# Performance work log

Hardware: AMD Instinct MI355X
Metric: run time of the kernel (lower is better)

The kernel has to match this reference:

```python
import jax, jax.numpy as jnp
import numpy as np

N_NODES = 50000
N_EDGES = 800000
D_FEAT = 128


def setup_inputs() -> dict:
    key = jax.random.key(0)
    k1, k2, k3, k4 = jax.random.split(key, 4)
    edge_index = jax.random.randint(k1, (2, N_EDGES), 0, N_NODES, dtype=jnp.int64 if jax.config.jax_enable_x64 else jnp.int32)
    edge_vals = jax.random.uniform(k2, (N_EDGES,), dtype=jnp.float32)
    features = jax.random.normal(k3, (N_NODES, D_FEAT), dtype=jnp.float32)
    bias = jax.random.normal(k4, (D_FEAT,), dtype=jnp.float32)
    return {"edge_index": edge_index, "edge_vals": edge_vals, "features": features, "bias": bias}


def reference(edge_index, edge_vals, features, bias):
    # SpMM: out[dst] += A[dst, src] * X[src], i.e. sparse adjacency @ dense features
    src = edge_index[0]
    dst = edge_index[1]
    msg = features[src] * edge_vals[:, None]          # [E, D] gather + scale
    out = jax.ops.segment_sum(msg, dst, num_segments=features.shape[0])  # [N, D] scatter-add
    return out + bias                                  # fused bias add
```

## Files before the change

kernel.cpp:

```cpp
#include <hip/hip_runtime.h>
#include <hip/hip_bf16.h>

#define D_FEAT 128
#define D4 (D_FEAT / 4)
#define BKT_SHIFT 7
#define BKT_NODES 128
#define NCHUNK 256
#define MAXBKT 512
#define MAXBSUM 128
#define CAP 3072

__global__ __launch_bounds__(256) void k1_hist_cvt(
        const int* __restrict__ dst, int E, int chunk, int nbkt,
        int* __restrict__ M, int Mpad,
        const float4* __restrict__ fin, __hip_bfloat162* __restrict__ fout,
        int n4) {
    int c = blockIdx.x;
    int tid = threadIdx.x;
    if (c < NCHUNK) {
        __shared__ int hist[MAXBKT];
        for (int i = tid; i < nbkt; i += 256) hist[i] = 0;
        __syncthreads();
        int lo = c * chunk;
        int hi = min(lo + chunk, E);
        for (int i = lo + tid; i < hi; i += 256)
            atomicAdd(&hist[dst[i] >> BKT_SHIFT], 1);
        __syncthreads();
        for (int i = tid; i < nbkt; i += 256)
            M[i * NCHUNK + c] = hist[i];
        if (c == 0) {
            for (int i = nbkt * NCHUNK + tid; i < Mpad; i += 256) M[i] = 0;
        }
    } else {
        int nb = gridDim.x - NCHUNK;
        int idx = (c - NCHUNK) * 256 + tid;
        int stride = nb * 256;
        for (int i = idx; i < n4; i += stride) {
            float4 f = fin[i];
            fout[2 * i + 0] = __float22bfloat162_rn(make_float2(f.x, f.y));
            fout[2 * i + 1] = __float22bfloat162_rn(make_float2(f.z, f.w));
        }
    }
}

__global__ __launch_bounds__(1024) void k2a_scan(int* __restrict__ M,
                                                 int* __restrict__ bsum) {
    __shared__ int s[1024];
    int tid = threadIdx.x;
    int j = blockIdx.x * 1024 + tid;
    int v = M[j];
    s[tid] = v;
    __syncthreads();
    for (int off = 1; off < 1024; off <<= 1) {
        int t = (tid >= off) ? s[tid - off] : 0;
        __syncthreads();
        s[tid] += t;
        __syncthreads();
    }
    M[j] = s[tid] - v;
    if (tid == 1023) bsum[blockIdx.x] = s[1023];
}

__device__ inline void scan_bsum_lds(const int* __restrict__ bsum, int nblk,
                                     int* sbs, int tid) {
    int v = 0;
    if (tid < MAXBSUM) {
        v = (tid < nblk) ? bsum[tid] : 0;
        sbs[tid] = v;
    }
    __syncthreads();
    for (int off = 1; off < MAXBSUM; off <<= 1) {
        int t = (tid < MAXBSUM && tid >= off) ? sbs[tid - off] : 0;
        __syncthreads();
        if (tid < MAXBSUM) sbs[tid] += t;
        __syncthreads();
    }
    if (tid < MAXBSUM) sbs[tid] -= v;
    __syncthreads();
}

__global__ __launch_bounds__(512) void k3_partition(
        const int* __restrict__ src, const int* __restrict__ dst,
        const float* __restrict__ vals, int E, int chunk, int nbkt, int nblk,
        const int* __restrict__ M, const int* __restrict__ bsum,
        int2* __restrict__ spackA) {
    __shared__ int sbs[MAXBSUM];
    __shared__ int lcur[MAXBKT];
    int c = blockIdx.x;
    int tid = threadIdx.x;
    scan_bsum_lds(bsum, nblk, sbs, tid);
    for (int i = tid; i < nbkt; i += 512) {
        int j = i * NCHUNK + c;
        lcur[i] = M[j] + sbs[j >> 10];
    }
    __syncthreads();
    int lo = c * chunk;
    int hi = min(lo + chunk, E);
    for (int i = lo + tid; i < hi; i += 512) {
        int d = dst[i];
        int s = src[i];
        float v = vals[i];
        int pos = atomicAdd(&lcur[d >> BKT_SHIFT], 1);
        spackA[pos] = make_int2((s & 0xFFFF) | ((d & (BKT_NODES - 1)) << 16),
                                __float_as_int(v));
    }
}

__global__ __launch_bounds__(1024) void k45_sort_gather(
        const int* __restrict__ M, const int* __restrict__ bsum, int nblk,
        const int2* __restrict__ spackA, int2* __restrict__ spackB,
        const __hip_bfloat162* __restrict__ feat,
        const float2* __restrict__ bias2, float2* __restrict__ out2,
        int N, int nbkt) {
    __shared__ int sbs[MAXBSUM];
    __shared__ int hist[BKT_NODES];
    __shared__ int sbuf[BKT_NODES];
    __shared__ int lcur[BKT_NODES];
    __shared__ int2 ls[CAP];
    int b = blockIdx.x;
    int tid = threadIdx.x;
    scan_bsum_lds(bsum, nblk, sbs, tid);
    int j0 = b * NCHUNK;
    int j1 = (b + 1) * NCHUNK;
    int base = M[j0] + sbs[j0 >> 10];
    int end  = M[j1] + sbs[j1 >> 10];
    int cnt = end - base;
    bool inlds = (cnt <= CAP);

    if (tid < BKT_NODES) hist[tid] = 0;
    __syncthreads();
    for (int i = tid; i < cnt; i += 1024)
        atomicAdd(&hist[(spackA[base + i].x >> 16) & (BKT_NODES - 1)], 1);
    __syncthreads();
    if (tid < BKT_NODES) sbuf[tid] = hist[tid];
    __syncthreads();
    for (int off = 1; off < BKT_NODES; off <<= 1) {
        int t = (tid < BKT_NODES && tid >= off) ? sbuf[tid - off] : 0;
        __syncthreads();
        if (tid < BKT_NODES) sbuf[tid] += t;
        __syncthreads();
    }
    if (tid < BKT_NODES) lcur[tid] = sbuf[tid] - hist[tid];
    __syncthreads();
    for (int i = tid; i < cnt; i += 1024) {
        int2 r = spackA[base + i];
        int p = atomicAdd(&lcur[(r.x >> 16) & (BKT_NODES - 1)], 1);
        if (inlds) ls[p] = r;
        else       spackB[base + p] = r;
    }
    __syncthreads();

    int wave = tid >> 6, lane = tid & 63;
    float2 bv = bias2[lane];
    for (int n = wave; n < BKT_NODES; n += 16) {
        int node = (b << BKT_SHIFT) + n;
        if (node >= N) break;
        int lbeg = sbuf[n] - hist[n];
        int lend = sbuf[n];
        float2 acc0 = bv;
        float2 acc1 = make_float2(0.f, 0.f);
        if (inlds) {
            for (int e0 = lbeg; e0 < lend; e0 += 8) {
                int2 p[8];
                __hip_bfloat162 h[8];
#pragma unroll
                for (int j = 0; j < 8; j++) p[j] = ls[min(e0 + j, lend - 1)];
#pragma unroll
                for (int j = 0; j < 8; j++)
                    h[j] = feat[(size_t)(p[j].x & 0xFFFF) * 64 + lane];
#pragma unroll
                for (int j = 0; j < 8; j++) {
                    float v = (e0 + j < lend) ? __int_as_float(p[j].y) : 0.f;
                    float2 f = __bfloat1622float2(h[j]);
                    if (j & 1) { acc1.x += v * f.x; acc1.y += v * f.y; }
                    else       { acc0.x += v * f.x; acc0.y += v * f.y; }
                }
            }
        } else {
            for (int e0 = lbeg; e0 < lend; e0 += 8) {
                int2 p[8];
                __hip_bfloat162 h[8];
#pragma unroll
                for (int j = 0; j < 8; j++)
                    p[j] = spackB[base + min(e0 + j, lend - 1)];
#pragma unroll
                for (int j = 0; j < 8; j++)
                    h[j] = feat[(size_t)(p[j].x & 0xFFFF) * 64 + lane];
#pragma unroll
                for (int j = 0; j < 8; j++) {
                    float v = (e0 + j < lend) ? __int_as_float(p[j].y) : 0.f;
                    float2 f = __bfloat1622float2(h[j]);
                    if (j & 1) { acc1.x += v * f.x; acc1.y += v * f.y; }
                    else       { acc0.x += v * f.x; acc0.y += v * f.y; }
                }
            }
        }
        acc0.x += acc1.x; acc0.y += acc1.y;
        out2[(size_t)node * 64 + lane] = acc0;
    }
}


__global__ void init_bias_kernel(float4* __restrict__ out,
                                 const float4* __restrict__ bias, int n4) {
    int i = blockIdx.x * blockDim.x + threadIdx.x;
    if (i < n4) out[i] = bias[i & (D4 - 1)];
}

__global__ void spmm_edge_kernel(const int* __restrict__ src,
                                 const int* __restrict__ dst,
                                 const float* __restrict__ vals,
                                 const float4* __restrict__ feat,
                                 float* __restrict__ out, int n_edges) {
    int tid = blockIdx.x * blockDim.x + threadIdx.x;
    int e = tid >> 5;
    int lane = tid & 31;
    if (e >= n_edges) return;
    int s = src[e];
    int d = dst[e];
    float v = vals[e];
    float4 f = feat[(size_t)s * D4 + lane];
    float* o = out + (size_t)d * D_FEAT + lane * 4;
    atomicAdd(o + 0, v * f.x);
    atomicAdd(o + 1, v * f.y);
    atomicAdd(o + 2, v * f.z);
    atomicAdd(o + 3, v * f.w);
}

extern "C" void kernel_launch(void* const* d_in, const int* in_sizes, int n_in,
                              void* d_out, int out_size, void* d_ws, size_t ws_size,
                              hipStream_t stream) {
    const int* edge_index = (const int*)d_in[0];
    const float* edge_vals = (const float*)d_in[1];
    const float* features  = (const float*)d_in[2];
    const float* bias      = (const float*)d_in[3];

    int E = in_sizes[1];
    int N = in_sizes[2] / D_FEAT;
    const int* src = edge_index;
    const int* dst = edge_index + E;
    float* out = (float*)d_out;

    int nbkt = (N + BKT_NODES - 1) >> BKT_SHIFT;
    int n4 = N * D_FEAT / 4;
    int chunk = (E + NCHUNK - 1) / NCHUNK;
    int Mpad = ((nbkt * NCHUNK + 1 + 1023) / 1024) * 1024;
    int nblk2 = Mpad / 1024;

    size_t fb_bytes = (size_t)N * D_FEAT * 2;
    size_t sp_bytes = (size_t)E * 8;
    size_t needed = fb_bytes + 2 * sp_bytes +
                    ((size_t)Mpad + nblk2) * 4;

    bool ok = (ws_size >= needed) && (N >= 1) && (N <= 65536) && (E >= 1) &&
              (in_sizes[3] == D_FEAT) && (nbkt <= MAXBKT) && (nblk2 <= MAXBSUM);

    if (ok) {
        char* wp = (char*)d_ws;
        __hip_bfloat162* fb16 = (__hip_bfloat162*)wp;  wp += fb_bytes;
        int2* spackA = (int2*)wp;                      wp += sp_bytes;
        int2* spackB = (int2*)wp;                      wp += sp_bytes;
        int* M       = (int*)wp;                       wp += (size_t)Mpad * 4;
        int* bsum    = (int*)wp;

        k1_hist_cvt<<<NCHUNK + 256, 256, 0, stream>>>(dst, E, chunk, nbkt,
                                                      M, Mpad,
                                                      (const float4*)features,
                                                      fb16, n4);
        k2a_scan<<<nblk2, 1024, 0, stream>>>(M, bsum);
        k3_partition<<<NCHUNK, 512, 0, stream>>>(src, dst, edge_vals, E, chunk,
                                                 nbkt, nblk2, M, bsum, spackA);
        k45_sort_gather<<<nbkt, 1024, 0, stream>>>(M, bsum, nblk2,
                                                   spackA, spackB,
                                                   fb16, (const float2*)bias,
                                                   (float2*)out, N, nbkt);
    } else {
        int no4 = out_size / 4;
        {
            int block = 256, grid = (no4 + block - 1) / block;
            init_bias_kernel<<<grid, block, 0, stream>>>((float4*)out,
                                                         (const float4*)bias, no4);
        }
        {
            int block = 256;
            long long total = (long long)E * 32;
            int grid = (int)((total + block - 1) / block);
            spmm_edge_kernel<<<grid, block, 0, stream>>>(src, dst, edge_vals,
                                                         (const float4*)features,
                                                         out, E);
        }
    }
}
```

Baseline: 146.0 us.

## Split wave into half-waves gathering 8-byte feature rows, use shuffle scans

In the gather phase each wave now splits into two 32-lane halves, and each half processes alternate edges. Each lane loads 4 bf16 features (8 bytes) instead of 2, and the halves are combined with a cross-half shuffle before the float4 store. This doubles the number of edges in flight per wave and widens memory transactions, at the cost of an extra reduction step. The LDS-based block scans of bucket sums and the per-node histogram are replaced with wave-level shuffle scans, which removes many barriers. The bf16 conversion also writes packed uint2 values.

Measured after the change: 144.1 us. No clear change (-1.3%).

```diff
diff --git a/kernel.cpp b/kernel.cpp
--- a/kernel.cpp
+++ b/kernel.cpp
@@ -10,10 +10,17 @@
 #define MAXBSUM 128
 #define CAP 3072
 
+__device__ inline unsigned pack_bf2(float lo, float hi) {
+    __hip_bfloat162 h = __float22bfloat162_rn(make_float2(lo, hi));
+    unsigned u;
+    __builtin_memcpy(&u, &h, 4);
+    return u;
+}
+
 __global__ __launch_bounds__(256) void k1_hist_cvt(
         const int* __restrict__ dst, int E, int chunk, int nbkt,
         int* __restrict__ M, int Mpad,
-        const float4* __restrict__ fin, __hip_bfloat162* __restrict__ fout,
+        const float4* __restrict__ fin, uint2* __restrict__ fout,
         int n4) {
     int c = blockIdx.x;
     int tid = threadIdx.x;
@@ -37,8 +44,10 @@
         int stride = nb * 256;
         for (int i = idx; i < n4; i += stride) {
             float4 f = fin[i];
-            fout[2 * i + 0] = __float22bfloat162_rn(make_float2(f.x, f.y));
-            fout[2 * i + 1] = __float22bfloat162_rn(make_float2(f.z, f.w));
+            uint2 o;
+            o.x = pack_bf2(f.x, f.y);
+            o.y = pack_bf2(f.z, f.w);
+            fout[i] = o;
         }
     }
 }
@@ -61,21 +70,21 @@
     if (tid == 1023) bsum[blockIdx.x] = s[1023];
 }
 
-__device__ inline void scan_bsum_lds(const int* __restrict__ bsum, int nblk,
-                                     int* sbs, int tid) {
-    int v = 0;
-    if (tid < MAXBSUM) {
-        v = (tid < nblk) ? bsum[tid] : 0;
-        sbs[tid] = v;
-    }
-    __syncthreads();
-    for (int off = 1; off < MAXBSUM; off <<= 1) {
-        int t = (tid < MAXBSUM && tid >= off) ? sbs[tid - off] : 0;
-        __syncthreads();
-        if (tid < MAXBSUM) sbs[tid] += t;
-        __syncthreads();
-    }
-    if (tid < MAXBSUM) sbs[tid] -= v;
+__device__ inline void scan_bsum_wave(const int* __restrict__ bsum, int nblk,
+                                      int* sbs, int tid) {
+    if (tid < 64) {
+        int i0 = 2 * tid, i1 = 2 * tid + 1;
+        int h0 = (i0 < nblk) ? bsum[i0] : 0;
+        int h1 = (i1 < nblk) ? bsum[i1] : 0;
+        int s = h0 + h1;
+        int v = s;
+        for (int off = 1; off < 64; off <<= 1) {
+            int t = __shfl_up(v, off, 64);
+            if (tid >= off) v += t;
+        }
+        sbs[i0] = v - s;
+        sbs[i1] = v - s + h0;
+    }
     __syncthreads();
 }
 
@@ -88,7 +97,7 @@
     __shared__ int lcur[MAXBKT];
     int c = blockIdx.x;
     int tid = threadIdx.x;
-    scan_bsum_lds(bsum, nblk, sbs, tid);
+    scan_bsum_wave(bsum, nblk, sbs, tid);
     for (int i = tid; i < nbkt; i += 512) {
         int j = i * NCHUNK + c;
         lcur[i] = M[j] + sbs[j >> 10];
@@ -109,8 +118,8 @@
 __global__ __launch_bounds__(1024) void k45_sort_gather(
         const int* __restrict__ M, const int* __restrict__ bsum, int nblk,
         const int2* __restrict__ spackA, int2* __restrict__ spackB,
-        const __hip_bfloat162* __restrict__ feat,
-        const float2* __restrict__ bias2, float2* __restrict__ out2,
+        const uint2* __restrict__ feat2,
+        const float4* __restrict__ bias4, float4* __restrict__ out4,
         int N, int nbkt) {
     __shared__ int sbs[MAXBSUM];
     __shared__ int hist[BKT_NODES];
@@ -119,7 +128,7 @@
     __shared__ int2 ls[CAP];
     int b = blockIdx.x;
     int tid = threadIdx.x;
-    scan_bsum_lds(bsum, nblk, sbs, tid);
+    scan_bsum_wave(bsum, nblk, sbs, tid);
     int j0 = b * NCHUNK;
     int j1 = (b + 1) * NCHUNK;
     int base = M[j0] + sbs[j0 >> 10];
@@ -132,15 +141,19 @@
     for (int i = tid; i < cnt; i += 1024)
         atomicAdd(&hist[(spackA[base + i].x >> 16) & (BKT_NODES - 1)], 1);
     __syncthreads();
-    if (tid < BKT_NODES) sbuf[tid] = hist[tid];
-    __syncthreads();
-    for (int off = 1; off < BKT_NODES; off <<= 1) {
-        int t = (tid < BKT_NODES && tid >= off) ? sbuf[tid - off] : 0;
-        __syncthreads();
-        if (tid < BKT_NODES) sbuf[tid] += t;
-        __syncthreads();
-    }
-    if (tid < BKT_NODES) lcur[tid] = sbuf[tid] - hist[tid];
+    if (tid < 64) {
+        int h0 = hist[2 * tid], h1 = hist[2 * tid + 1];
+        int s = h0 + h1;
+        int v = s;
+        for (int off = 1; off < 64; off <<= 1) {
+            int t = __shfl_up(v, off, 64);
+            if (tid >= off) v += t;
+        }
+        sbuf[2 * tid]     = v - h1;
+        sbuf[2 * tid + 1] = v;
+        lcur[2 * tid]     = v - s;
+        lcur[2 * tid + 1] = v - h1;
+    }
     __syncthreads();
     for (int i = tid; i < cnt; i += 1024) {
         int2 r = spackA[base + i];
@@ -151,52 +164,82 @@
     __syncthreads();
 
     int wave = tid >> 6, lane = tid & 63;
-    float2 bv = bias2[lane];
+    int half = lane >> 5;
+    int hl   = lane & 31;
+    float4 bv = bias4[hl];
     for (int n = wave; n < BKT_NODES; n += 16) {
         int node = (b << BKT_SHIFT) + n;
         if (node >= N) break;
-        int lbeg = sbuf[n] - hist[n];
         int lend = sbuf[n];
-        float2 acc0 = bv;
-        float2 acc1 = make_float2(0.f, 0.f);
+        int lbeg = lend - hist[n];
+        float4 acc0 = make_float4(0.f, 0.f, 0.f, 0.f);
+        float4 acc1 = make_float4(0.f, 0.f, 0.f, 0.f);
         if (inlds) {
-            for (int e0 = lbeg; e0 < lend; e0 += 8) {
+            for (int e0 = lbeg; e0 < lend; e0 += 16) {
                 int2 p[8];
-                __hip_bfloat162 h[8];
-#pragma unroll
-                for (int j = 0; j < 8; j++) p[j] = ls[min(e0 + j, lend - 1)];
+                uint2 h[8];
 #pragma unroll
                 for (int j = 0; j < 8; j++)
-                    h[j] = feat[(size_t)(p[j].x & 0xFFFF) * 64 + lane];
+                    p[j] = ls[min(e0 + 2 * j + half, lend - 1)];
+#pragma unroll
+                for (int j = 0; j < 8; j++)
+                    h[j] = feat2[(size_t)(p[j].x & 0xFFFF) * 32 + hl];
 #pragma unroll
                 for (int j = 0; j < 8; j++) {
-                    float v = (e0 + j < lend) ? __int_as_float(p[j].y) : 0.f;
-                    float2 f = __bfloat1622float2(h[j]);
-                    if (j & 1) { acc1.x += v * f.x; acc1.y += v * f.y; }
-                    else       { acc0.x += v * f.x; acc0.y += v * f.y; }
+                    float v = (e0 + 2 * j + half < lend) ? __int_as_float(p[j].y) : 0.f;
+                    __hip_bfloat162 blo, bhi;
+                    __builtin_memcpy(&blo, &h[j].x, 4);
+                    __builtin_memcpy(&bhi, &h[j].y, 4);
+                    float2 f01 = __bfloat1622float2(blo);
+                    float2 f23 = __bfloat1622float2(bhi);
+                    if (j & 1) {
+                        acc1.x += v * f01.x; acc1.y += v * f01.y;
+                        acc1.z += v * f23.x; acc1.w += v * f23.y;
+                    } else {
+                        acc0.x += v * f01.x; acc0.y += v * f01.y;
+                        acc0.z += v * f23.x; acc0.w += v * f23.y;
+                    }
                 }
             }
         } else {
-            for (int e0 = lbeg; e0 < lend; e0 += 8) {
+            for (int e0 = lbeg; e0 < lend; e0 += 16) {
                 int2 p[8];
-                __hip_bfloat162 h[8];
+                uint2 h[8];
 #pragma unroll
                 for (int j = 0; j < 8; j++)
-                    p[j] = spackB[base + min(e0 + j, lend - 1)];
+                    p[j] = spackB[base + min(e0 + 2 * j + half, lend - 1)];
 #pragma unroll
                 for (int j = 0; j < 8; j++)
-                    h[j] = feat[(size_t)(p[j].x & 0xFFFF) * 64 + lane];
+                    h[j] = feat2[(size_t)(p[j].x & 0xFFFF) * 32 + hl];
 #pragma unroll
                 for (int j = 0; j < 8; j++) {
-                    float v = (e0 + j < lend) ? __int_as_float(p[j].y) : 0.f;
-                    float2 f = __bfloat1622float2(h[j]);
-                    if (j & 1) { acc1.x += v * f.x; acc1.y += v * f.y; }
-                    else       { acc0.x += v * f.x; acc0.y += v * f.y; }
+                    float v = (e0 + 2 * j + half < lend) ? __int_as_float(p[j].y) : 0.f;
+                    __hip_bfloat162 blo, bhi;
+                    __builtin_memcpy(&blo, &h[j].x, 4);
+                    __builtin_memcpy(&bhi, &h[j].y, 4);
+                    float2 f01 = __bfloat1622float2(blo);
+                    float2 f23 = __bfloat1622float2(bhi);
+                    if (j & 1) {
+                        acc1.x += v * f01.x; acc1.y += v * f01.y;
+                        acc1.z += v * f23.x; acc1.w += v * f23.y;
+                    } else {
+                        acc0.x += v * f01.x; acc0.y += v * f01.y;
+                        acc0.z += v * f23.x; acc0.w += v * f23.y;
+                    }
                 }
             }
         }
         acc0.x += acc1.x; acc0.y += acc1.y;
-        out2[(size_t)node * 64 + lane] = acc0;
+        acc0.z += acc1.z; acc0.w += acc1.w;
+        acc0.x += __shfl_xor(acc0.x, 32);
+        acc0.y += __shfl_xor(acc0.y, 32);
+        acc0.z += __shfl_xor(acc0.z, 32);
+        acc0.w += __shfl_xor(acc0.w, 32);
+        if (half == 0) {
+            out4[(size_t)node * 32 + hl] =
+                make_float4(acc0.x + bv.x, acc0.y + bv.y,
+                            acc0.z + bv.z, acc0.w + bv.w);
+        }
     }
 }
 
@@ -257,7 +300,7 @@
 
     if (ok) {
         char* wp = (char*)d_ws;
-        __hip_bfloat162* fb16 = (__hip_bfloat162*)wp;  wp += fb_bytes;
+        uint2* fb16 = (uint2*)wp;                      wp += fb_bytes;
         int2* spackA = (int2*)wp;                      wp += sp_bytes;
         int2* spackB = (int2*)wp;                      wp += sp_bytes;
         int* M       = (int*)wp;                       wp += (size_t)Mpad * 4;
@@ -272,8 +315,9 @@
                                                  nbkt, nblk2, M, bsum, spackA);
         k45_sort_gather<<<nbkt, 1024, 0, stream>>>(M, bsum, nblk2,
                                                    spackA, spackB,
-                                                   fb16, (const float2*)bias,
-                                                   (float2*)out, N, nbkt);
+                                                   (const uint2*)fb16,
+                                                   (const float4*)bias,
+                                                   (float4*)out, N, nbkt);
     } else {
         int no4 = out_size / 4;
         {
```
